# Kernel tuning notes

Measured on AMD Instinct MI355X. Metric: run time of the kernel, lower is better.

## Reference

```python
import jax, jax.numpy as jnp
import numpy as np

NUM_CLASSES = 80
STRIDES = (8, 16, 32)


def _decode(p, stride):
    # p: [B, 5+C, H, W] raw head -> [B, HW, 5+C] decoded (xy in px, wh=exp*stride)
    B, C, H, W = p.shape
    ys, xs = jnp.meshgrid(jnp.arange(H), jnp.arange(W), indexing='ij')
    grid = jnp.stack([xs, ys], -1).reshape(H * W, 2).astype(p.dtype)
    out = p.reshape(B, C, H * W).transpose(0, 2, 1)
    xy = (out[..., :2] + grid) * stride
    wh = jnp.exp(out[..., 2:4]) * stride
    out = jnp.concatenate([xy, wh, out[..., 4:]], -1)
    es = jnp.full((H * W,), float(stride), p.dtype)
    return out, grid[:, 0], grid[:, 1], es


def _pairwise_iou(gt, pr):
    # gt [G,4] cxcywh, pr [A,4] -> [G,A]
    gt_tl = gt[:, None, :2] - gt[:, None, 2:] * 0.5
    gt_br = gt[:, None, :2] + gt[:, None, 2:] * 0.5
    pr_tl = pr[None, :, :2] - pr[None, :, 2:] * 0.5
    pr_br = pr[None, :, :2] + pr[None, :, 2:] * 0.5
    tl = jnp.maximum(gt_tl, pr_tl)
    br = jnp.minimum(gt_br, pr_br)
    en = jnp.all(tl < br, -1).astype(gt.dtype)
    inter = jnp.prod(br - tl, -1) * en
    a_gt = jnp.prod(gt[:, 2:], -1)[:, None]
    a_pr = jnp.prod(pr[:, 2:], -1)[None, :]
    return inter / (a_gt + a_pr - inter + 1e-16)


def _assign(gt_boxes, gt_cls, bbox, clsp, objp, xg, yg, es):
    # SimOTA assignment for one image (all fixed-shape; non-candidate anchors
    # are masked out via huge cost instead of boolean gather).
    G = gt_boxes.shape[0]
    xc = (xg + 0.5) * es  # [A] anchor centers
    yc = (yg + 0.5) * es
    gl = gt_boxes[:, 0:1] - 0.5 * gt_boxes[:, 2:3]
    gr = gt_boxes[:, 0:1] + 0.5 * gt_boxes[:, 2:3]
    gt_ = gt_boxes[:, 1:2] - 0.5 * gt_boxes[:, 3:4]
    gb = gt_boxes[:, 1:2] + 0.5 * gt_boxes[:, 3:4]
    in_box = (xc[None] > gl) & (xc[None] < gr) & (yc[None] > gt_) & (yc[None] < gb)  # [G,A]
    r = 2.5 * es[None]
    in_ctr = ((xc[None] > gt_boxes[:, 0:1] - r) & (xc[None] < gt_boxes[:, 0:1] + r)
              & (yc[None] > gt_boxes[:, 1:2] - r) & (yc[None] < gt_boxes[:, 1:2] + r))
    fg_cand = jnp.any(in_box, 0) | jnp.any(in_ctr, 0)  # [A]
    in_both = in_box & in_ctr  # [G,A]

    ious = _pairwise_iou(gt_boxes, bbox)  # [G,A]
    ious_m = jnp.where(fg_cand[None, :], ious, 0.0)
    iou_cost = -jnp.log(ious_m + 1e-8)

    # pairwise cls BCE cost: bce(sqrt(sigmoid(cls)*sigmoid(obj)), onehot(gt)).sum(-1)
    p = jnp.sqrt(jax.nn.sigmoid(clsp) * jax.nn.sigmoid(objp[:, None]))  # [A,C]
    lp = jnp.maximum(jnp.log(p), -100.0)
    l1p = jnp.maximum(jnp.log1p(-p), -100.0)
    t = jax.nn.one_hot(gt_cls, NUM_CLASSES, dtype=p.dtype)  # [G,C]
    cls_cost = -(jnp.einsum('ac,gc->ga', lp - l1p, t) + jnp.sum(l1p, -1)[None, :])

    cost = (cls_cost + 3.0 * iou_cost
            + 1e5 * (~in_both).astype(p.dtype)
            + 1e9 * (~fg_cand)[None, :].astype(p.dtype))

    # dynamic-k: k_g = clamp(sum(top10 ious), min=1)
    topk_ious, _ = jax.lax.top_k(ious_m, 10)
    dyn_k = jnp.clip(topk_ious.sum(-1).astype(jnp.int32), 1, None)  # [G]
    rank = jnp.argsort(jnp.argsort(cost, axis=1), axis=1)  # rank of each anchor per gt
    matching = (rank < dyn_k[:, None]) & fg_cand[None, :]  # [G,A]
    # resolve anchors matched to multiple gts: keep min-cost gt
    multi = matching.sum(0) > 1
    best = jnp.argmin(cost, 0)
    matching = jnp.where(multi[None, :], jnp.arange(G)[:, None] == best[None, :], matching)

    fg = jnp.any(matching, 0)  # [A]
    matched_gt = jnp.argmax(matching, 0)  # [A]
    pred_iou = jnp.sum(matching * ious, 0)  # [A]
    matched_cls = gt_cls[matched_gt]
    return fg, matched_gt, pred_iou, matched_cls


def _giou_loss(b, g):
    tl = jnp.maximum(b[..., :2] - b[..., 2:] * 0.5, g[..., :2] - g[..., 2:] * 0.5)
    br = jnp.minimum(b[..., :2] + b[..., 2:] * 0.5, g[..., :2] + g[..., 2:] * 0.5)
    area_b = jnp.prod(b[..., 2:], -1)
    area_g = jnp.prod(g[..., 2:], -1)
    en = jnp.all(tl < br, -1).astype(b.dtype)
    inter = jnp.prod(br - tl, -1) * en
    union = area_b + area_g - inter
    iou = inter / (union + 1e-16)
    ctl = jnp.minimum(b[..., :2] - b[..., 2:] * 0.5, g[..., :2] - g[..., 2:] * 0.5)
    cbr = jnp.maximum(b[..., :2] + b[..., 2:] * 0.5, g[..., :2] + g[..., 2:] * 0.5)
    area_c = jnp.maximum(jnp.prod(cbr - ctl, -1), 1e-16)
    giou = iou - (area_c - union) / area_c
    return 1.0 - jnp.clip(giou, -1.0, 1.0)


def _bce_logits(x, t):
    return jnp.maximum(x, 0.0) - x * t + jnp.log1p(jnp.exp(-jnp.abs(x)))


def _forward(p8, p16, p32, labels):
    outs, xo, yo, eo = [], [], [], []
    for p, s in zip((p8, p16, p32), STRIDES):
        o, x, y, e = _decode(p, s)
        outs.append(o); xo.append(x); yo.append(y); eo.append(e)
    outputs = jnp.concatenate(outs, 1)  # [B, A, 5+C]
    xg = jnp.concatenate(xo); yg = jnp.concatenate(yo); es = jnp.concatenate(eo)

    bbox = outputs[..., :4]
    obj = outputs[..., 4]
    cls = outputs[..., 5:]
    gt_boxes = labels[..., :4]
    gt_cls = labels[..., 4].astype(jnp.int32)

    # assignment runs under no_grad in torch
    det = jax.lax.stop_gradient(outputs)
    fg, matched_gt, pred_iou, matched_cls = jax.vmap(
        lambda gb, gc, o: _assign(gb, gc, o[..., :4], o[..., 5:], o[..., 4], xg, yg, es)
    )(gt_boxes, gt_cls, det)

    fgf = fg.astype(outputs.dtype)  # [B,A]
    reg_t = jnp.take_along_axis(gt_boxes, matched_gt[..., None], axis=1)  # [B,A,4]
    cls_t = (jax.nn.one_hot(matched_cls, NUM_CLASSES, dtype=outputs.dtype)
             * pred_iou[..., None] * fgf[..., None])

    loss_iou = jnp.sum(_giou_loss(bbox, reg_t) * fgf)
    loss_obj = jnp.sum(_bce_logits(obj, fgf))
    loss_cls = jnp.sum(_bce_logits(cls, cls_t) * fgf[..., None])
    num_fg = jnp.maximum(jnp.sum(fgf), 1.0)
    return (5.0 * loss_iou + loss_obj + loss_cls) / num_fg


def setup_inputs() -> dict:
    key = jax.random.key(0)
    k1, k2, k3, k4, k5, k6 = jax.random.split(key, 6)
    B, NGT = 32, 20
    p8 = jax.random.normal(k1, (B, 5 + NUM_CLASSES, 80, 80), dtype=jnp.float32)
    p16 = jax.random.normal(k2, (B, 5 + NUM_CLASSES, 40, 40), dtype=jnp.float32)
    p32 = jax.random.normal(k3, (B, 5 + NUM_CLASSES, 20, 20), dtype=jnp.float32)
    cxy = jax.random.uniform(k4, (B, NGT, 2), dtype=jnp.float32, minval=32.0, maxval=608.0)
    wh = jax.random.uniform(k5, (B, NGT, 2), dtype=jnp.float32, minval=16.0, maxval=128.0)
    cls = jax.random.randint(k6, (B, NGT, 1), 0, NUM_CLASSES).astype(jnp.float32)
    labels = jnp.concatenate([cxy, wh, cls], -1)
    return {"p8": p8, "p16": p16, "p32": p32, "labels": labels}


def reference(p8, p16, p32, labels):
    return _forward(p8, p16, p32, labels)
```

## Files before the change

### kernel.cpp

```cpp
#include <hip/hip_runtime.h>
#include <cstdint>
#include <cstddef>

#define NA 8400
#define NAP 8448
#define NB 32
#define NG 20
#define NCL 80
#define NBLK 33
#define PSPL 4

__device__ __forceinline__ float frcp(float x) { return __builtin_amdgcn_rcpf(x); }
__device__ __forceinline__ float bce0(float x) {
  return fmaxf(x, 0.0f) + __logf(1.0f + __expf(-fabsf(x)));
}

__device__ __forceinline__ void anchor_info(int a, const float* p8, const float* p16,
                                            const float* p32, int b, const float*& base,
                                            int& hw, int& HW, int& xg, int& yg, float& fs) {
  if (a < 6400)      { hw = a;        HW = 6400; xg = hw % 80; yg = hw / 80; fs = 8.f;
                       base = p8  + (size_t)b * 85 * 6400; }
  else if (a < 8000) { hw = a - 6400; HW = 1600; xg = hw % 40; yg = hw / 40; fs = 16.f;
                       base = p16 + (size_t)b * 85 * 1600; }
  else               { hw = a - 8000; HW = 400;  xg = hw % 20; yg = hw / 20; fs = 32.f;
                       base = p32 + (size_t)b * 85 * 400; }
}

__device__ __forceinline__ float iou_raw(float gx, float gy, float gw, float gh, float4 p) {
  float gtlx = gx - gw * 0.5f, gtly = gy - gh * 0.5f;
  float gbrx = gx + gw * 0.5f, gbry = gy + gh * 0.5f;
  float ptlx = p.x - p.z * 0.5f, ptly = p.y - p.w * 0.5f;
  float pbrx = p.x + p.z * 0.5f, pbry = p.y + p.w * 0.5f;
  float tlx = fmaxf(gtlx, ptlx), tly = fmaxf(gtly, ptly);
  float brx = fminf(gbrx, pbrx), bry = fminf(gbry, pbry);
  float inter = ((tlx < brx) && (tly < bry)) ? (brx - tlx) * (bry - tly) : 0.0f;
  float ag = gw * gh, ap = p.z * p.w;
  return inter * frcp(ag + ap - inter + 1e-16f);
}

__device__ __forceinline__ float giou_loss(float4 bb, float gx, float gy, float gw, float gh) {
  float btlx = bb.x - bb.z * 0.5f, btly = bb.y - bb.w * 0.5f;
  float bbrx = bb.x + bb.z * 0.5f, bbry = bb.y + bb.w * 0.5f;
  float gtlx = gx - gw * 0.5f, gtly = gy - gh * 0.5f;
  float gbrx = gx + gw * 0.5f, gbry = gy + gh * 0.5f;
  float tlx = fmaxf(btlx, gtlx), tly = fmaxf(btly, gtly);
  float brx = fminf(bbrx, gbrx), bry = fminf(bbry, gbry);
  float area_b = bb.z * bb.w, area_g = gw * gh;
  float inter = ((tlx < brx) && (tly < bry)) ? (brx - tlx) * (bry - tly) : 0.0f;
  float uni = area_b + area_g - inter;
  float iou = inter / (uni + 1e-16f);
  float ctlx = fminf(btlx, gtlx), ctly = fminf(btly, gtly);
  float cbrx = fmaxf(bbrx, gbrx), cbry = fmaxf(bbry, gbry);
  float area_c = fmaxf((cbrx - ctlx) * (cbry - ctly), 1e-16f);
  float giou = iou - (area_c - uni) / area_c;
  giou = fminf(fmaxf(giou, -1.0f), 1.0f);
  return 1.0f - giou;
}

__global__ __launch_bounds__(256) void k1(const float* __restrict__ p8,
                                          const float* __restrict__ p16,
                                          const float* __restrict__ p32,
                                          const float* __restrict__ labels,
                                          int* __restrict__ n_fg_cnt,
                                          int* __restrict__ fg_list,
                                          unsigned int* __restrict__ am_c,
                                          float4* __restrict__ bbox_c,
                                          float* __restrict__ lso_c,
                                          unsigned int* __restrict__ match_c,
                                          float* __restrict__ blk_obj) {
  __shared__ float s_gt[NG * 4];
  __shared__ unsigned int s_wcnt[4];
  __shared__ float s_part[4];
  __shared__ unsigned int s_base;
  int blk = blockIdx.x, b = blockIdx.y, tid = threadIdx.x, lane = tid & 63, wid = tid >> 6;

  if (tid < NG) {
    s_gt[tid * 4 + 0] = labels[((size_t)b * NG + tid) * 5 + 0];
    s_gt[tid * 4 + 1] = labels[((size_t)b * NG + tid) * 5 + 1];
    s_gt[tid * 4 + 2] = labels[((size_t)b * NG + tid) * 5 + 2];
    s_gt[tid * 4 + 3] = labels[((size_t)b * NG + tid) * 5 + 3];
  }
  __syncthreads();

  int a = blk * 256 + tid;
  match_c[(size_t)b * NAP + a] = 0u;

  bool fg = false;
  unsigned int msk = 0u;
  float bce_obj = 0.0f, obj = 0.0f;
  const float* base = nullptr; int hw = 0, HW = 0, xg = 0, yg = 0; float fs = 8.f;
  if (a < NA) {
    anchor_info(a, p8, p16, p32, b, base, hw, HW, xg, yg, fs);
    obj = base[4 * HW + hw];
    bce_obj = bce0(obj);
    float xc = ((float)xg + 0.5f) * fs;
    float yc = ((float)yg + 0.5f) * fs;
    float r = 2.5f * fs;
#pragma unroll
    for (int g = 0; g < NG; ++g) {
      float gx = s_gt[g * 4 + 0], gy = s_gt[g * 4 + 1];
      float gw = s_gt[g * 4 + 2], gh = s_gt[g * 4 + 3];
      bool inb = (xc > gx - 0.5f * gw) && (xc < gx + 0.5f * gw) &&
                 (yc > gy - 0.5f * gh) && (yc < gy + 0.5f * gh);
      bool inc = (xc > gx - r) && (xc < gx + r) && (yc > gy - r) && (yc < gy + r);
      fg = fg || inb || inc;
      if (inb && inc) msk |= (1u << g);
    }
  }

  unsigned long long bm = __ballot(fg);
#pragma unroll
  for (int off = 32; off; off >>= 1) bce_obj += __shfl_down(bce_obj, off, 64);
  if (lane == 0) { s_wcnt[wid] = (unsigned int)__popcll(bm); s_part[wid] = bce_obj; }
  __syncthreads();
  if (tid == 0) {
    unsigned int cnt = s_wcnt[0] + s_wcnt[1] + s_wcnt[2] + s_wcnt[3];
    s_base = cnt ? (unsigned int)atomicAdd(&n_fg_cnt[b], (int)cnt) : 0u;
    blk_obj[b * NBLK + blk] = s_part[0] + s_part[1] + s_part[2] + s_part[3];
  }
  __syncthreads();

  if (!fg) return;
  unsigned int pos = s_base;
  for (int w = 0; w < wid; ++w) pos += s_wcnt[w];
  pos += (unsigned int)__popcll(bm & ((1ull << lane) - 1ull));
  size_t bo = (size_t)b * NAP;
  int ci = (int)pos;
  fg_list[bo + ci] = a;
  am_c[bo + ci] = msk;

  float v0 = base[hw];
  float v1 = base[HW + hw];
  float v2 = base[2 * HW + hw];
  float v3 = base[3 * HW + hw];
  bbox_c[bo + ci] = make_float4((v0 + (float)xg) * fs, (v1 + (float)yg) * fs,
                                __expf(v2) * fs, __expf(v3) * fs);
  float uo = __logf(1.0f + __expf(-fabsf(obj)));
  lso_c[bo + ci] = fminf(obj, 0.0f) - uo;
}

__global__ __launch_bounds__(256) void k23(const float* __restrict__ p8,
                                           const float* __restrict__ p16,
                                           const float* __restrict__ p32,
                                           const float* __restrict__ labels,
                                           const int* __restrict__ fg_list,
                                           const int* __restrict__ n_fg,
                                           const float* __restrict__ lso_c,
                                           const unsigned int* __restrict__ am_c,
                                           const float4* __restrict__ bbox_c,
                                           float* __restrict__ sb_c,
                                           float2* __restrict__ ct_tbl) {
  __shared__ float s_gt[NG * 4];
  __shared__ int   s_gcls[NG];
  __shared__ float s_sl[8][33];
  __shared__ float s_sb[8][33];
  __shared__ float s_slr[32];
  int b = blockIdx.y, tid = threadIdx.x;
  int part = tid >> 5, cl = tid & 31;

  if (tid < NG) {
    s_gt[tid * 4 + 0] = labels[((size_t)b * NG + tid) * 5 + 0];
    s_gt[tid * 4 + 1] = labels[((size_t)b * NG + tid) * 5 + 1];
    s_gt[tid * 4 + 2] = labels[((size_t)b * NG + tid) * 5 + 2];
    s_gt[tid * 4 + 3] = labels[((size_t)b * NG + tid) * 5 + 3];
    s_gcls[tid] = (int)labels[((size_t)b * NG + tid) * 5 + 4];
  }
  __syncthreads();

  int n = n_fg[b];
  size_t bo = (size_t)b * NAP;

  for (int base_ci = blockIdx.x * 32; base_ci < n; base_ci += gridDim.x * 32) {
    int ci = base_ci + cl;
    bool act = ci < n;
    const float* base = nullptr; int hw = 0, HW = 0, xg, yg; float fs;
    float lso = 0.0f, sl = 0.0f, sb = 0.0f;
    if (act) {
      int a = fg_list[bo + ci];
      lso = lso_c[bo + ci];
      anchor_info(a, p8, p16, p32, b, base, hw, HW, xg, yg, fs);
      const float* cb = base + (size_t)(5 + part * 10) * HW + hw;
      float xs[10];
#pragma unroll
      for (int j = 0; j < 10; ++j) xs[j] = cb[(size_t)j * HW];
#pragma unroll
      for (int j = 0; j < 10; ++j) {
        float x = xs[j];
        float u = __logf(1.0f + __expf(-fabsf(x)));
        sb += fmaxf(x, 0.0f) + u;
        float lsx = fminf(x, 0.0f) - u;
        float lpr = 0.5f * (lsx + lso);
        float p   = __expf(lpr);
        sl += fmaxf(__logf(1.0f - p), -100.0f);
      }
    }
    s_sl[part][cl] = sl;
    s_sb[part][cl] = sb;
    __syncthreads();
    if (tid < 32) {
      float tsl = 0.0f, tsb = 0.0f;
#pragma unroll
      for (int q = 0; q < 8; ++q) { tsl += s_sl[q][tid]; tsb += s_sb[q][tid]; }
      s_slr[tid] = tsl;
      if (base_ci + tid < n) sb_c[bo + base_ci + tid] = tsb;
    }
    __syncthreads();
    if (act) {
      float slr = s_slr[cl];
      unsigned int am = am_c[bo + ci];
      float4 pb = bbox_c[bo + ci];
#pragma unroll
      for (int gg = 0; gg < 3; ++gg) {
        int g = part + (gg << 3);
        if (g < NG) {
          int cg = s_gcls[g];
          float x = base[(size_t)(5 + cg) * HW + hw];
          float u = __logf(1.0f + __expf(-fabsf(x)));
          float lsx = fminf(x, 0.0f) - u;
          float lpr = 0.5f * (lsx + lso);
          float p   = __expf(lpr);
          float l1p = fmaxf(__logf(1.0f - p), -100.0f);
          float wv  = fmaxf(lpr, -100.0f) - l1p;
          float iou = iou_raw(s_gt[g * 4 + 0], s_gt[g * 4 + 1],
                              s_gt[g * 4 + 2], s_gt[g * 4 + 3], pb);
          float cst = -(wv + slr) - 3.0f * __logf(iou + 1e-8f);
          if (!((am >> g) & 1u)) cst += 100000.0f;
          ct_tbl[((size_t)b * NG + g) * NAP + ci] = make_float2(cst, iou);
        }
      }
    }
    __syncthreads();
  }
}

__global__ __launch_bounds__(256) void kBC(const float2* __restrict__ ct_tbl,
                                           const int* __restrict__ n_fg,
                                           float* __restrict__ scr_iou,
                                           float* __restrict__ scr_cst,
                                           int* __restrict__ scr_ci) {
  __shared__ float s_wt[4 * 10];
  __shared__ float s_wc[4 * 10];
  __shared__ int   s_wi[4 * 10];
  int p = blockIdx.x, g = blockIdx.y, b = blockIdx.z;
  int tid = threadIdx.x, lane = tid & 63, wid = tid >> 6;
  int n = n_fg[b];
  const float2* __restrict__ row = ct_tbl + ((size_t)b * NG + g) * NAP;

  float t10[10];
  float c10v[10];
  int   c10i[10];
#pragma unroll
  for (int j = 0; j < 10; ++j) { t10[j] = 0.0f; c10v[j] = 3.4e38f; c10i[j] = 0x7fffffff; }

  for (int ci = p * 256 + tid; ci < n; ci += PSPL * 256) {
    float2 e = row[ci];
    float cst = e.x, iou = e.y;
    if (iou > t10[9]) {
      t10[9] = iou;
#pragma unroll
      for (int q = 9; q > 0; --q) {
        if (t10[q] > t10[q - 1]) { float t = t10[q]; t10[q] = t10[q - 1]; t10[q - 1] = t; }
        else break;
      }
    }
    if (cst < c10v[9] || (cst == c10v[9] && ci < c10i[9])) {
      c10v[9] = cst; c10i[9] = ci;
#pragma unroll
      for (int q = 9; q > 0; --q) {
        if (c10v[q] < c10v[q - 1] ||
            (c10v[q] == c10v[q - 1] && c10i[q] < c10i[q - 1])) {
          float tv = c10v[q]; c10v[q] = c10v[q - 1]; c10v[q - 1] = tv;
          int   ti = c10i[q]; c10i[q] = c10i[q - 1]; c10i[q - 1] = ti;
        } else break;
      }
    }
  }

  for (int r = 0; r < 10; ++r) {
    float v = t10[0];
    float bv = v;
    float cv = c10v[0]; int cix = c10i[0];
    float cbv = cv;     int cbi = cix;
#pragma unroll
    for (int off = 32; off; off >>= 1) {
      bv = fmaxf(bv, __shfl_down(bv, off, 64));
      float ov = __shfl_down(cbv, off, 64);
      int   oi = __shfl_down(cbi, off, 64);
      if (ov < cbv || (ov == cbv && oi < cbi)) { cbv = ov; cbi = oi; }
    }
    bv  = __shfl(bv, 0, 64);
    cbv = __shfl(cbv, 0, 64);
    cbi = __shfl(cbi, 0, 64);
    unsigned long long won = __ballot(v == bv);
    if (lane == __ffsll(won) - 1) {
#pragma unroll
      for (int q = 0; q < 9; ++q) t10[q] = t10[q + 1];
      t10[9] = -1.0f;
    }
    if (cv == cbv && cix == cbi) {
#pragma unroll
      for (int q = 0; q < 9; ++q) { c10v[q] = c10v[q + 1]; c10i[q] = c10i[q + 1]; }
      c10v[9] = 3.4e38f; c10i[9] = 0x7fffffff;
    }
    if (lane == 0) {
      s_wt[wid * 10 + r] = bv;
      s_wc[wid * 10 + r] = cbv;
      s_wi[wid * 10 + r] = cbi;
    }
  }
  __syncthreads();

  if (tid == 0) {
    int obase = (((b * NG + g) * PSPL) + p) * 10;
    int p0 = 0, p1 = 0, p2 = 0, p3 = 0;
    for (int r = 0; r < 10; ++r) {
      float v0 = (p0 < 10) ? s_wt[p0]      : -2.0f;
      float v1 = (p1 < 10) ? s_wt[10 + p1] : -2.0f;
      float v2 = (p2 < 10) ? s_wt[20 + p2] : -2.0f;
      float v3 = (p3 < 10) ? s_wt[30 + p3] : -2.0f;
      float m = fmaxf(fmaxf(v0, v1), fmaxf(v2, v3));
      scr_iou[obase + r] = m;
      if (m == v0) ++p0; else if (m == v1) ++p1; else if (m == v2) ++p2; else ++p3;
    }
    int q[4] = {0, 0, 0, 0};
    for (int r = 0; r < 10; ++r) {
      float bv = 0.0f; int bi = 0; int sel = -1;
#pragma unroll
      for (int w = 0; w < 4; ++w) {
        if (q[w] < 10) {
          float v = s_wc[w * 10 + q[w]];
          int   i = s_wi[w * 10 + q[w]];
          if (sel < 0 || v < bv || (v == bv && i < bi)) { bv = v; bi = i; sel = w; }
        }
      }
      scr_cst[obase + r] = bv;
      scr_ci[obase + r]  = bi;
      ++q[sel];
    }
  }
}

__global__ __launch_bounds__(64) void kM(const float* __restrict__ scr_iou,
                                         const float* __restrict__ scr_cst,
                                         const int* __restrict__ scr_ci,
                                         unsigned int* __restrict__ match_c) {
  int g = blockIdx.x, b = blockIdx.y, lane = threadIdx.x;
  int bg = b * NG + g;
  float v;
  float cv; int cix;
  if (lane < PSPL * 10) {
    v   = scr_iou[bg * (PSPL * 10) + lane];
    cv  = scr_cst[bg * (PSPL * 10) + lane];
    cix = scr_ci [bg * (PSPL * 10) + lane];
  } else {
    v = -1.0f; cv = 3.4e38f; cix = 0x7fffffff;
  }

  float s = 0.0f;
  for (int r = 0; r < 10; ++r) {
    float bv = v;
#pragma unroll
    for (int off = 32; off; off >>= 1) bv = fmaxf(bv, __shfl_down(bv, off, 64));
    bv = __shfl(bv, 0, 64);
    s += bv;
    unsigned long long won = __ballot(v == bv);
    if (lane == __ffsll(won) - 1) v = -1.0f;
  }
  int k = (int)s;
  if (k < 1) k = 1;

  size_t bo = (size_t)b * NAP;
  for (int it = 0; it < k; ++it) {
    float cbv = cv; int cbi = cix;
#pragma unroll
    for (int off = 32; off; off >>= 1) {
      float ov = __shfl_down(cbv, off, 64);
      int   oi = __shfl_down(cbi, off, 64);
      if (ov < cbv || (ov == cbv && oi < cbi)) { cbv = ov; cbi = oi; }
    }
    cbv = __shfl(cbv, 0, 64);
    cbi = __shfl(cbi, 0, 64);
    if (cbv >= 1e37f) break;
    unsigned long long won = __ballot(cv == cbv && cix == cbi);
    if (lane == __ffsll(won) - 1) {
      atomicOr(&match_c[bo + cbi], 1u << g);
      cv = 3.4e38f; cix = 0x7fffffff;
    }
  }
}

__global__ __launch_bounds__(256) void kD(const float* __restrict__ p8,
                                          const float* __restrict__ p16,
                                          const float* __restrict__ p32,
                                          const float* __restrict__ labels,
                                          const float2* __restrict__ ct_tbl,
                                          const int* __restrict__ n_fg,
                                          const unsigned int* __restrict__ match_c,
                                          const int* __restrict__ fg_list,
                                          const float4* __restrict__ bbox_c,
                                          const float* __restrict__ sb_c,
                                          const float* __restrict__ blk_obj,
                                          float* __restrict__ accum,
                                          int* __restrict__ done,
                                          float* __restrict__ out) {
  __shared__ float s_gt[NG * 5];
  __shared__ float s_red[16];
  __shared__ int s_flag;
  int b = blockIdx.y, tid = threadIdx.x;
  int n = n_fg[b];
  size_t bo = (size_t)b * NAP;

  if (tid < NG * 5) s_gt[tid] = labels[(size_t)b * NG * 5 + tid];
  __syncthreads();

  float li = 0.0f, oe = 0.0f, lc = 0.0f, nf = 0.0f;
  int ci = blockIdx.x * 256 + tid;
  if (ci < n) {
    unsigned int m = match_c[bo + ci];
    if (m != 0u) {
      int mg;
      if (m & (m - 1)) {
        float bestc = 3.4e38f; mg = 0;
#pragma unroll 4
        for (int gq = 0; gq < NG; ++gq) {
          float cst = ct_tbl[((size_t)b * NG + gq) * NAP + ci].x;
          if (cst < bestc) { bestc = cst; mg = gq; }
        }
      } else {
        mg = __ffs(m) - 1;
      }
      int a = fg_list[bo + ci];
      const float* base; int hw, HW, xg, yg; float fs;
      anchor_info(a, p8, p16, p32, b, base, hw, HW, xg, yg, fs);
      float4 pb = bbox_c[bo + ci];
      float gx = s_gt[mg * 5], gy = s_gt[mg * 5 + 1];
      float gw = s_gt[mg * 5 + 2], gh = s_gt[mg * 5 + 3];
      int cgq = (int)s_gt[mg * 5 + 4];
      float piou = ct_tbl[((size_t)b * NG + mg) * NAP + ci].y;
      li = giou_loss(pb, gx, gy, gw, gh);
      float xcls = base[(size_t)(5 + cgq) * HW + hw];
      lc = sb_c[bo + ci] - xcls * piou;
      oe = base[4 * HW + hw];
      nf = 1.0f;
    }
  }

  float vals[4] = {li, oe, lc, nf};
#pragma unroll
  for (int q2 = 0; q2 < 4; ++q2) {
#pragma unroll
    for (int off = 32; off; off >>= 1) vals[q2] += __shfl_down(vals[q2], off, 64);
  }
  int lane = tid & 63;
  if (lane == 0) {
    int w = tid >> 6;
    s_red[w * 4 + 0] = vals[0];
    s_red[w * 4 + 1] = vals[1];
    s_red[w * 4 + 2] = vals[2];
    s_red[w * 4 + 3] = vals[3];
  }
  __syncthreads();
  if (tid < 4) {
    const int slot[4] = {0, 2, 3, 4};
    float s = s_red[tid] + s_red[4 + tid] + s_red[8 + tid] + s_red[12 + tid];
    if (s != 0.0f) atomicAdd(&accum[slot[tid]], s);
  }
  __syncthreads();

  if (tid == 0) {
    __threadfence();
    s_flag = (atomicAdd(done, 1) == NBLK * NB - 1) ? 1 : 0;
  }
  __syncthreads();
  if (!s_flag) return;

  float s = 0.0f;
  for (int i = tid; i < NB * NBLK; i += 256) s += blk_obj[i];
#pragma unroll
  for (int off = 32; off; off >>= 1) s += __shfl_down(s, off, 64);
  if ((tid & 63) == 0) s_red[tid >> 6] = s;
  __syncthreads();
  if (tid == 0) {
    float obj_base = s_red[0] + s_red[1] + s_red[2] + s_red[3];
    float loss_iou = atomicAdd(&accum[0], 0.0f);
    float oex      = atomicAdd(&accum[2], 0.0f);
    float loss_cls = atomicAdd(&accum[3], 0.0f);
    float num_fg   = atomicAdd(&accum[4], 0.0f);
    float loss_obj = obj_base - oex;
    out[0] = (5.0f * loss_iou + loss_obj + loss_cls) / fmaxf(num_fg, 1.0f);
  }
}

extern "C" void kernel_launch(void* const* d_in, const int* in_sizes, int n_in,
                              void* d_out, int out_size, void* d_ws, size_t ws_size,
                              hipStream_t stream) {
  const float* p8     = (const float*)d_in[0];
  const float* p16    = (const float*)d_in[1];
  const float* p32    = (const float*)d_in[2];
  const float* labels = (const float*)d_in[3];
  float* out = (float*)d_out;

  const size_t BAP = (size_t)NB * NAP;
  char* w = (char*)d_ws;
  float4*       bbox_c   = (float4*)w;
  float2*       ct_tbl   = (float2*)(w + BAP * 16);
  char*         w2       = (char*)ct_tbl + (size_t)NB * NG * NAP * 8;
  int*          fg_list  = (int*)(w2);
  unsigned int* match_c  = (unsigned int*)(w2 + BAP * 4);
  float*        sb_c     = (float*)(w2 + BAP * 8);
  float*        lso_c    = (float*)(w2 + BAP * 12);
  unsigned int* am_c     = (unsigned int*)(w2 + BAP * 16);
  char*         w3       = w2 + BAP * 20;
  int*          n_fg     = (int*)w3;
  float*        accum    = (float*)(w3 + 128);
  int*          done     = (int*)(w3 + 384);
  float*        blk_obj  = (float*)(w3 + 512);
  char*         scr      = w3 + 8192;
  float*        scr_iou  = (float*)scr;
  float*        scr_cst  = (float*)(scr + 102400);
  int*          scr_ci   = (int*)  (scr + 204800);

  hipMemsetAsync(w3, 0, 512, stream);

  k1 <<<dim3(NBLK, NB), dim3(256), 0, stream>>>(p8, p16, p32, labels, n_fg, fg_list, am_c,
                                                bbox_c, lso_c, match_c, blk_obj);
  k23<<<dim3(NBLK, NB), dim3(256), 0, stream>>>(p8, p16, p32, labels, fg_list, n_fg, lso_c,
                                                am_c, bbox_c, sb_c, ct_tbl);
  kBC<<<dim3(PSPL, NG, NB), dim3(256), 0, stream>>>(ct_tbl, n_fg, scr_iou, scr_cst, scr_ci);
  kM <<<dim3(NG, NB), dim3(64), 0, stream>>>(scr_iou, scr_cst, scr_ci, match_c);
  kD <<<dim3(NBLK, NB), dim3(256), 0, stream>>>(p8, p16, p32, labels, ct_tbl, n_fg, match_c,
                                                fg_list, bbox_c, sb_c, blk_obj, accum,
                                                done, out);
}
```

Measured before the change: 207.4 us.

## Fuse top-k partial selection and matching kernels into one block per gt

Merges the partitioned top-10 scan (kBC) and the matching kernel (kM) into a single kernel, with one 256-thread block per (gt, image) scanning the whole candidate row. The block computes dynamic k and sets the match bits directly, so the scratch buffers and one kernel launch go away. The cost is 4x fewer blocks for the scan, so each block does 4x more serial work over the candidate list. Parallelism in that stage drops in exchange for less launch and global round-trip overhead.

New measurement: 189.7 us. -8.6%, faster.

```diff
diff --git a/kernel.cpp b/kernel.cpp
--- a/kernel.cpp
+++ b/kernel.cpp
@@ -8,7 +8,6 @@
 #define NG 20
 #define NCL 80
 #define NBLK 33
-#define PSPL 4
 
 __device__ __forceinline__ float frcp(float x) { return __builtin_amdgcn_rcpf(x); }
 __device__ __forceinline__ float bce0(float x) {
@@ -233,17 +232,16 @@
   }
 }
 
-__global__ __launch_bounds__(256) void kBC(const float2* __restrict__ ct_tbl,
-                                           const int* __restrict__ n_fg,
-                                           float* __restrict__ scr_iou,
-                                           float* __restrict__ scr_cst,
-                                           int* __restrict__ scr_ci) {
+__global__ __launch_bounds__(256) void kBCM(const float2* __restrict__ ct_tbl,
+                                            const int* __restrict__ n_fg,
+                                            unsigned int* __restrict__ match_c) {
   __shared__ float s_wt[4 * 10];
   __shared__ float s_wc[4 * 10];
   __shared__ int   s_wi[4 * 10];
-  int p = blockIdx.x, g = blockIdx.y, b = blockIdx.z;
-  int tid = threadIdx.x, lane = tid & 63, wid = tid >> 6;
+  int g = blockIdx.x, b = blockIdx.y, tid = threadIdx.x;
+  int lane = tid & 63, wid = tid >> 6;
   int n = n_fg[b];
+  size_t bo = (size_t)b * NAP;
   const float2* __restrict__ row = ct_tbl + ((size_t)b * NG + g) * NAP;
 
   float t10[10];
@@ -252,7 +250,7 @@
 #pragma unroll
   for (int j = 0; j < 10; ++j) { t10[j] = 0.0f; c10v[j] = 3.4e38f; c10i[j] = 0x7fffffff; }
 
-  for (int ci = p * 256 + tid; ci < n; ci += PSPL * 256) {
+  for (int ci = tid; ci < n; ci += 256) {
     float2 e = row[ci];
     float cst = e.x, iou = e.y;
     if (iou > t10[9]) {
@@ -311,80 +309,33 @@
   __syncthreads();
 
   if (tid == 0) {
-    int obase = (((b * NG + g) * PSPL) + p) * 10;
     int p0 = 0, p1 = 0, p2 = 0, p3 = 0;
+    float s = 0.0f;
     for (int r = 0; r < 10; ++r) {
       float v0 = (p0 < 10) ? s_wt[p0]      : -2.0f;
       float v1 = (p1 < 10) ? s_wt[10 + p1] : -2.0f;
       float v2 = (p2 < 10) ? s_wt[20 + p2] : -2.0f;
       float v3 = (p3 < 10) ? s_wt[30 + p3] : -2.0f;
       float m = fmaxf(fmaxf(v0, v1), fmaxf(v2, v3));
-      scr_iou[obase + r] = m;
+      s += m;
       if (m == v0) ++p0; else if (m == v1) ++p1; else if (m == v2) ++p2; else ++p3;
     }
+    int k = (int)s;
+    if (k < 1) k = 1;
     int q[4] = {0, 0, 0, 0};
-    for (int r = 0; r < 10; ++r) {
-      float bv = 0.0f; int bi = 0; int sel = -1;
+    for (int it = 0; it < k; ++it) {
+      float bv = 3.3e38f; int bi = 0x7fffffff; int sel = -1;
 #pragma unroll
       for (int w = 0; w < 4; ++w) {
         if (q[w] < 10) {
           float v = s_wc[w * 10 + q[w]];
           int   i = s_wi[w * 10 + q[w]];
-          if (sel < 0 || v < bv || (v == bv && i < bi)) { bv = v; bi = i; sel = w; }
+          if (v < bv || (v == bv && i < bi)) { bv = v; bi = i; sel = w; }
         }
       }
-      scr_cst[obase + r] = bv;
-      scr_ci[obase + r]  = bi;
+      if (sel < 0 || bv >= 1e37f) break;
+      atomicOr(&match_c[bo + bi], 1u << g);
       ++q[sel];
-    }
-  }
-}
-
-__global__ __launch_bounds__(64) void kM(const float* __restrict__ scr_iou,
-                                         const float* __restrict__ scr_cst,
-                                         const int* __restrict__ scr_ci,
-                                         unsigned int* __restrict__ match_c) {
-  int g = blockIdx.x, b = blockIdx.y, lane = threadIdx.x;
-  int bg = b * NG + g;
-  float v;
-  float cv; int cix;
-  if (lane < PSPL * 10) {
-    v   = scr_iou[bg * (PSPL * 10) + lane];
-    cv  = scr_cst[bg * (PSPL * 10) + lane];
-    cix = scr_ci [bg * (PSPL * 10) + lane];
-  } else {
-    v = -1.0f; cv = 3.4e38f; cix = 0x7fffffff;
-  }
-
-  float s = 0.0f;
-  for (int r = 0; r < 10; ++r) {
-    float bv = v;
-#pragma unroll
-    for (int off = 32; off; off >>= 1) bv = fmaxf(bv, __shfl_down(bv, off, 64));
-    bv = __shfl(bv, 0, 64);
-    s += bv;
-    unsigned long long won = __ballot(v == bv);
-    if (lane == __ffsll(won) - 1) v = -1.0f;
-  }
-  int k = (int)s;
-  if (k < 1) k = 1;
-
-  size_t bo = (size_t)b * NAP;
-  for (int it = 0; it < k; ++it) {
-    float cbv = cv; int cbi = cix;
-#pragma unroll
-    for (int off = 32; off; off >>= 1) {
-      float ov = __shfl_down(cbv, off, 64);
-      int   oi = __shfl_down(cbi, off, 64);
-      if (ov < cbv || (ov == cbv && oi < cbi)) { cbv = ov; cbi = oi; }
-    }
-    cbv = __shfl(cbv, 0, 64);
-    cbi = __shfl(cbi, 0, 64);
-    if (cbv >= 1e37f) break;
-    unsigned long long won = __ballot(cv == cbv && cix == cbi);
-    if (lane == __ffsll(won) - 1) {
-      atomicOr(&match_c[bo + cbi], 1u << g);
-      cv = 3.4e38f; cix = 0x7fffffff;
     }
   }
 }
@@ -515,20 +466,15 @@
   float*        accum    = (float*)(w3 + 128);
   int*          done     = (int*)(w3 + 384);
   float*        blk_obj  = (float*)(w3 + 512);
-  char*         scr      = w3 + 8192;
-  float*        scr_iou  = (float*)scr;
-  float*        scr_cst  = (float*)(scr + 102400);
-  int*          scr_ci   = (int*)  (scr + 204800);
 
   hipMemsetAsync(w3, 0, 512, stream);
 
-  k1 <<<dim3(NBLK, NB), dim3(256), 0, stream>>>(p8, p16, p32, labels, n_fg, fg_list, am_c,
-                                                bbox_c, lso_c, match_c, blk_obj);
-  k23<<<dim3(NBLK, NB), dim3(256), 0, stream>>>(p8, p16, p32, labels, fg_list, n_fg, lso_c,
-                                                am_c, bbox_c, sb_c, ct_tbl);
-  kBC<<<dim3(PSPL, NG, NB), dim3(256), 0, stream>>>(ct_tbl, n_fg, scr_iou, scr_cst, scr_ci);
-  kM <<<dim3(NG, NB), dim3(64), 0, stream>>>(scr_iou, scr_cst, scr_ci, match_c);
-  kD <<<dim3(NBLK, NB), dim3(256), 0, stream>>>(p8, p16, p32, labels, ct_tbl, n_fg, match_c,
-                                                fg_list, bbox_c, sb_c, blk_obj, accum,
-                                                done, out);
-}
+  k1  <<<dim3(NBLK, NB), dim3(256), 0, stream>>>(p8, p16, p32, labels, n_fg, fg_list, am_c,
+                                                 bbox_c, lso_c, match_c, blk_obj);
+  k23 <<<dim3(NBLK, NB), dim3(256), 0, stream>>>(p8, p16, p32, labels, fg_list, n_fg, lso_c,
+                                                 am_c, bbox_c, sb_c, ct_tbl);
+  kBCM<<<dim3(NG, NB), dim3(256), 0, stream>>>(ct_tbl, n_fg, match_c);
+  kD  <<<dim3(NBLK, NB), dim3(256), 0, stream>>>(p8, p16, p32, labels, ct_tbl, n_fg, match_c,
+                                                 fg_list, bbox_c, sb_c, blk_obj, accum,
+                                                 done, out);
+}
```
